# Kernel optimization log

Hardware: AMD Instinct MI355X
Metric: run time of the kernel (lower is better)

## Reference

```python
import jax, jax.numpy as jnp
import numpy as np

E = 8        # num_experts
TOPK = 2     # k
D = 1024     # input/output size
H = 4096     # expert hidden size


def setup_inputs() -> dict:
    key = jax.random.key(0)
    ks = jax.random.split(key, 8)
    s = 0.02
    return {
        "hidden_states": jax.random.normal(ks[0], (2, 2048, D), dtype=jnp.float32),
        "Wr": jax.random.normal(ks[1], (D, E), dtype=jnp.float32) * s,
        "br": jnp.zeros((E,), dtype=jnp.float32),
        "gate_bias": jnp.zeros((E,), dtype=jnp.float32),
        "W1": jax.random.normal(ks[2], (E, D, H), dtype=jnp.float32) * s,
        "b1": jnp.zeros((E, H), dtype=jnp.float32),
        "W2": jax.random.normal(ks[3], (E, H, D), dtype=jnp.float32) * s,
        "b2": jnp.zeros((E, D), dtype=jnp.float32),
    }


def reference(hidden_states, Wr, br, gate_bias, W1, b1, W2, b2):
    B, S, Din = hidden_states.shape
    x = hidden_states.reshape(B * S, Din)              # [T, D]
    # Router: logits + gate bias, top-k, softmax over the k selected logits
    logits = x @ Wr + br + gate_bias                   # [T, E]
    top_v, top_i = jax.lax.top_k(logits, TOPK)         # [T, k]
    probs = jax.nn.softmax(top_v, axis=-1)             # [T, k]
    # Scatter top-k probs into dense per-expert gate weights [T, E]
    gate = jnp.einsum("tk,tke->te", probs,
                      jax.nn.one_hot(top_i, E, dtype=probs.dtype))
    # Per-expert MLP (exact gelu, eval mode -> no dropout/noise),
    # weighted-combine; zero gate weight == token not routed to expert.
    out = jnp.zeros((B * S, W2.shape[-1]), dtype=x.dtype)
    for e in range(E):
        h = jax.nn.gelu(x @ W1[e] + b1[e], approximate=False)  # [T, H]
        y = h @ W2[e] + b2[e]                                  # [T, D]
        out = out + gate[:, e:e + 1] * y
    return out.reshape(B, S, -1)
```

## Files before the change

kernel.cpp:

```cpp
#include <hip/hip_runtime.h>
#include <hip/hip_bf16.h>
#include <stdint.h>
#include <stddef.h>


#define T_TOK 4096
#define DIM   1024
#define HID   4096
#define NE    8
#define MT_MAX 40

typedef unsigned short u16;
typedef __bf16 bf16x8 __attribute__((ext_vector_type(8)));
typedef float  f32x4  __attribute__((ext_vector_type(4)));
typedef u16    u16x8  __attribute__((ext_vector_type(8)));

__device__ __forceinline__ u16 f2bf(float f) {
  union { float f; uint32_t u; } v; v.f = f;
  uint32_t u = v.u;
  return (u16)((u + 0x7fffu + ((u >> 16) & 1u)) >> 16);
}

__device__ __forceinline__ void async_load16(const void* g, void* l) {
  typedef __attribute__((address_space(1))) void GPtr;
  typedef __attribute__((address_space(3))) void LPtr;
  __builtin_amdgcn_global_load_lds((GPtr*)g, (LPtr*)l, 16, 0, 0);
}

__global__ void router_kernel(const float* __restrict__ x, const float* __restrict__ Wr,
                              const float* __restrict__ br, const float* __restrict__ gb,
                              int* __restrict__ counts, int* __restrict__ lists,
                              float* __restrict__ gate_p) {
  const int t = blockIdx.x * 4 + (threadIdx.x >> 6);
  const int lane = threadIdx.x & 63;
  const float* xr = x + (size_t)t * DIM;
  float acc[NE];
#pragma unroll
  for (int e = 0; e < NE; ++e) acc[e] = 0.f;
#pragma unroll
  for (int i = 0; i < DIM / 64; ++i) {
    const int k = i * 64 + lane;
    const float xv = xr[k];
    const float4 w0 = *reinterpret_cast<const float4*>(Wr + (size_t)k * NE);
    const float4 w1 = *reinterpret_cast<const float4*>(Wr + (size_t)k * NE + 4);
    acc[0] += xv * w0.x; acc[1] += xv * w0.y; acc[2] += xv * w0.z; acc[3] += xv * w0.w;
    acc[4] += xv * w1.x; acc[5] += xv * w1.y; acc[6] += xv * w1.z; acc[7] += xv * w1.w;
  }
#pragma unroll
  for (int off = 32; off >= 1; off >>= 1) {
#pragma unroll
    for (int e = 0; e < NE; ++e) acc[e] += __shfl_xor(acc[e], off);
  }
  if (lane == 0) {
    float lg[NE];
#pragma unroll
    for (int e = 0; e < NE; ++e) lg[e] = acc[e] + br[e] + gb[e];
    int i0 = 0;
#pragma unroll
    for (int e = 1; e < NE; ++e) if (lg[e] > lg[i0]) i0 = e;
    int i1 = (i0 == 0) ? 1 : 0;
#pragma unroll
    for (int e = 0; e < NE; ++e) if (e != i0 && lg[e] > lg[i1]) i1 = e;
    const float ev = expf(lg[i1] - lg[i0]);
    const float p0 = 1.f / (1.f + ev);
    const float p1 = ev / (1.f + ev);
    const int pos0 = atomicAdd(&counts[i0], 1);
    lists[i0 * T_TOK + pos0] = t * 2 + 0;
    const int pos1 = atomicAdd(&counts[i1], 1);
    lists[i1 * T_TOK + pos1] = t * 2 + 1;
    gate_p[t * 2 + 0] = p0;
    gate_p[t * 2 + 1] = p1;
  }
}

__global__ void tile_table_kernel(const int* __restrict__ counts, int* __restrict__ tab) {
  if (threadIdx.x == 0) {
    int tot = 0;
    for (int e = 0; e < NE; ++e) {
      const int c = counts[e];
      const int nt = (c + 255) >> 8;
      for (int i = 0; i < nt && tot < MT_MAX; ++i) {
        tab[tot * 2] = e; tab[tot * 2 + 1] = i * 256; ++tot;
      }
    }
    for (; tot < MT_MAX; ++tot) tab[tot * 2] = -1;
  }
}

__global__ void cvt_x_kernel(const float* __restrict__ in, u16* __restrict__ out, int n8) {
  const int i = blockIdx.x * blockDim.x + threadIdx.x;
  if (i >= n8) return;
  const float4 a = reinterpret_cast<const float4*>(in)[2 * i];
  const float4 b = reinterpret_cast<const float4*>(in)[2 * i + 1];
  u16x8 r;
  r[0] = f2bf(a.x); r[1] = f2bf(a.y); r[2] = f2bf(a.z); r[3] = f2bf(a.w);
  r[4] = f2bf(b.x); r[5] = f2bf(b.y); r[6] = f2bf(b.z); r[7] = f2bf(b.w);
  *reinterpret_cast<u16x8*>(out + (size_t)i * 8) = r;
}

__global__ void cvt_w_kernel(const float* __restrict__ in, u16* __restrict__ out,
                             int K, int N) {
  __shared__ float tile[64][65];
  const int e = blockIdx.z;
  const int n0 = blockIdx.x * 64, k0 = blockIdx.y * 64;
  const int tid = threadIdx.x;
  const float* src = in + (size_t)e * K * N;
#pragma unroll
  for (int r = 0; r < 16; ++r) {
    const int kr = r * 4 + (tid >> 6);
    tile[kr][tid & 63] = src[(size_t)(k0 + kr) * N + n0 + (tid & 63)];
  }
  __syncthreads();
  u16* dst = out + (size_t)e * N * K;
#pragma unroll
  for (int r = 0; r < 8; ++r) {
    const int nr = r * 8 + (tid >> 5);
    const int kc = (tid & 31) * 2;
    ushort2 v;
    v.x = f2bf(tile[kc][nr]);
    v.y = f2bf(tile[kc + 1][nr]);
    *reinterpret_cast<ushort2*>(&dst[(size_t)(n0 + nr) * K + k0 + kc]) = v;
  }
}

template <int KT, int NT, int NSPLIT, int PHASE>
__global__ __launch_bounds__(512, 2)
void gemm_kernel(const u16* __restrict__ Abase, const u16* __restrict__ Bt,
                 const float* __restrict__ bias, const int* __restrict__ counts,
                 const int* __restrict__ lists, const float* __restrict__ gate_p,
                 const int* __restrict__ tab,
                 u16* __restrict__ hout, float* __restrict__ yout) {
  const int e = tab[blockIdx.x * 2];
  if (e < 0) return;
  const int m0 = tab[blockIdx.x * 2 + 1];
  const int cnt = counts[e];
  const int n0 = blockIdx.y * 256;
  const int z = blockIdx.z;
  const int kbase = z * (KT / NSPLIT);
  constexpr int nkt = (KT / NSPLIT) / 64;
  constexpr int niter = nkt / 2;

  const int tid = threadIdx.x;
  const int lane = tid & 63, w = tid >> 6;
  const int wm = w >> 2, wn = w & 3;
  const int bh = wn >> 1, bs = wn & 1;
  const int l15 = lane & 15, lks = lane >> 4;

  __shared__ alignas(16) u16 lds[65536];
  __shared__ int rowp[256];

  if (tid < 256) {
    const int idx = m0 + tid;
    rowp[tid] = lists[e * T_TOK + (idx < cnt ? idx : cnt - 1)];
  }
  __syncthreads();

  const int sslot = (tid & 7) ^ ((tid >> 3) & 7);
  const u16* aPtr[2][2];
  const u16* bPtr[2][2];
#pragma unroll
  for (int h = 0; h < 2; ++h)
#pragma unroll
    for (int s = 0; s < 2; ++s) {
      const int r = h * 128 + s * 64 + (tid >> 3);
      const int p = rowp[r];
      const int arow = (PHASE == 1) ? (p >> 1) : p;
      aPtr[h][s] = Abase + (size_t)arow * KT + kbase + sslot * 8;
      bPtr[h][s] = Bt + ((size_t)e * NT + n0 + r) * KT + kbase + sslot * 8;
    }

  int aoff[2];
#pragma unroll
  for (int k = 0; k < 2; ++k)
    aoff[k] = l15 * 64 + (((k * 4 + lks) ^ (l15 & 7)) * 8);

  f32x4 acc[8][4];
#pragma unroll
  for (int a = 0; a < 8; ++a)
#pragma unroll
    for (int b = 0; b < 4; ++b) acc[a][b] = f32x4{0.f, 0.f, 0.f, 0.f};

  bf16x8 af[4][2], bfr[4][2];

#define RDA(C, FMH)                                                            \
  _Pragma("unroll") for (int f_ = 0; f_ < 4; ++f_)                             \
  _Pragma("unroll") for (int k_ = 0; k_ < 2; ++k_)                             \
    af[f_][k_] = *reinterpret_cast<const bf16x8*>(                             \
        &lds[(((C) * 2 + wm) * 2 + (FMH)) * 4096 + f_ * 1024 + aoff[k_]]);

#define RDB(C)                                                                 \
  _Pragma("unroll") for (int g_ = 0; g_ < 4; ++g_)                             \
  _Pragma("unroll") for (int k_ = 0; k_ < 2; ++k_)                             \
    bfr[g_][k_] = *reinterpret_cast<const bf16x8*>(                            \
        &lds[32768 + (((C) * 2 + bh) * 2 + bs) * 4096 + g_ * 1024 + aoff[k_]]);

#define SGA(C, S, TT)                                                          \
  _Pragma("unroll") for (int h_ = 0; h_ < 2; ++h_)                             \
    async_load16(aPtr[h_][S] + (TT) * 64,                                      \
                 &lds[(((C) * 2 + h_) * 2 + (S)) * 4096 + w * 512]);

#define SGB(C, H, TT)                                                          \
  _Pragma("unroll") for (int s_ = 0; s_ < 2; ++s_)                             \
    async_load16(bPtr[H][s_] + (TT) * 64,                                      \
                 &lds[32768 + (((C) * 2 + (H)) * 2 + s_) * 4096 + w * 512]);

#define MMQ(FMH, FNH)                                                          \
  _Pragma("unroll") for (int f_ = 0; f_ < 4; ++f_)                             \
  _Pragma("unroll") for (int g_ = 0; g_ < 2; ++g_)                             \
  _Pragma("unroll") for (int k_ = 0; k_ < 2; ++k_)                             \
    acc[(FMH) * 4 + f_][(FNH) * 2 + g_] =                                      \
        __builtin_amdgcn_mfma_f32_16x16x32_bf16(                               \
            af[f_][k_], bfr[(FNH) * 2 + g_][k_],                               \
            acc[(FMH) * 4 + f_][(FNH) * 2 + g_], 0, 0, 0);

#define CORE(FMH, FNH)                                                         \
  __builtin_amdgcn_s_barrier();                                                \
  asm volatile("s_waitcnt lgkmcnt(0)" ::: "memory");                           \
  __builtin_amdgcn_sched_barrier(0);                                           \
  __builtin_amdgcn_s_setprio(1);                                               \
  MMQ(FMH, FNH);                                                               \
  __builtin_amdgcn_s_setprio(0);                                               \
  __builtin_amdgcn_sched_barrier(0);

#define BAR() __builtin_amdgcn_s_barrier();

#define ITER(T, LAST)                                                          \
  {                                                                            \
    RDA(0, 0); RDB(0);                                                         \
    SGA(1, 1, (T) + 1);                                 \
    CORE(0, 0) BAR()                                                           \
    if (!(LAST)) { SGA(0, 0, (T) + 2); }                \
    CORE(0, 1) BAR()                                                           \
    RDA(0, 1);                                                                 \
    if (!(LAST)) { SGB(0, 0, (T) + 2); }                        \
    CORE(1, 0) BAR()                                                           \
    if (!(LAST)) { SGB(0, 1, (T) + 2); }                        \
    CORE(1, 1)                                                                 \
    if (LAST) { asm volatile("s_waitcnt vmcnt(0)" ::: "memory"); }             \
    else      { asm volatile("s_waitcnt vmcnt(6)" ::: "memory"); }             \
    __builtin_amdgcn_sched_barrier(0);                                         \
    BAR()                                                                      \
    RDA(1, 0); RDB(1);                                                         \
    if (!(LAST)) { SGA(0, 1, (T) + 2); }                        \
    CORE(0, 0) BAR()                                                           \
    if (!(LAST)) { SGA(1, 0, (T) + 3); }                \
    CORE(0, 1) BAR()                                                           \
    RDA(1, 1);                                                                 \
    if (!(LAST)) { SGB(1, 0, (T) + 3); }                        \
    CORE(1, 0) BAR()                                                           \
    if (!(LAST)) { SGB(1, 1, (T) + 3); }                        \
    CORE(1, 1)                                                                 \
    if (!(LAST)) {                                                             \
      asm volatile("s_waitcnt vmcnt(6)" ::: "memory");                         \
      __builtin_amdgcn_sched_barrier(0);                                       \
    }                                                                          \
    BAR()                                                                      \
  }

  SGA(0, 0, 0); SGB(0, 0, 0); SGB(0, 1, 0); SGA(0, 1, 0);
  SGA(1, 0, 1); SGB(1, 0, 1); SGB(1, 1, 1);
  asm volatile("s_waitcnt vmcnt(6)" ::: "memory");
  __builtin_amdgcn_sched_barrier(0);
  __builtin_amdgcn_s_barrier();

  for (int it = 0; it < niter - 1; ++it) {
    const int t = 2 * it;
    ITER(t, false);
  }
  ITER(nkt - 2, true);

#undef ITER
#undef CORE
#undef MMQ
#undef SGB
#undef SGA
#undef RDB
#undef RDA
#undef BAR

  const float* bias_e = bias + (size_t)e * NT;
  const float bz = (z == 0) ? 1.f : 0.f;
#pragma unroll
  for (int fm = 0; fm < 8; ++fm) {
    const int rbase = wm * 128 + (fm >> 2) * 64 + (fm & 3) * 16 + (lane >> 4) * 4;
#pragma unroll
    for (int r = 0; r < 4; ++r) {
      const int row = rbase + r;
      if (m0 + row >= cnt) continue;
      const int p = rowp[row];
#pragma unroll
      for (int nf = 0; nf < 4; ++nf) {
        const int n = n0 + wn * 64 + nf * 16 + l15;
        const float v = acc[fm][nf][r];
        if (PHASE == 1) {
          const float vb = v + bias_e[n];
          const float g = 0.5f * vb * (1.0f + erff(vb * 0.70710678118654752f));
          hout[(size_t)p * NT + n] = f2bf(g);
        } else if (PHASE == 2) {
          yout[(size_t)z * T_TOK * 2 * NT + (size_t)p * NT + n] =
              gate_p[p] * (v + bz * bias_e[n]);
        } else {
          atomicAdd(&yout[(size_t)(p >> 1) * NT + n], gate_p[p] * (v + bz * bias_e[n]));
        }
      }
    }
  }
}

__global__ void combine4_kernel(const float* __restrict__ yp, float* __restrict__ out) {
  const int i = blockIdx.x * blockDim.x + threadIdx.x;
  const int t = i >> 8, d4 = i & 255;
  const size_t r0 = (size_t)(2 * t) * 256 + d4;
  const size_t zoff = (size_t)T_TOK * 2 * DIM / 4;
  const float4 a = reinterpret_cast<const float4*>(yp)[r0];
  const float4 b = reinterpret_cast<const float4*>(yp)[r0 + 256];
  const float4 c = reinterpret_cast<const float4*>(yp)[zoff + r0];
  const float4 d = reinterpret_cast<const float4*>(yp)[zoff + r0 + 256];
  float4 o;
  o.x = a.x + b.x + c.x + d.x; o.y = a.y + b.y + c.y + d.y;
  o.z = a.z + b.z + c.z + d.z; o.w = a.w + b.w + c.w + d.w;
  reinterpret_cast<float4*>(out)[i] = o;
}

extern "C" void kernel_launch(void* const* d_in, const int* in_sizes, int n_in,
                              void* d_out, int out_size, void* d_ws, size_t ws_size,
                              hipStream_t stream) {
  const float* x  = (const float*)d_in[0];
  const float* Wr = (const float*)d_in[1];
  const float* br = (const float*)d_in[2];
  const float* gb = (const float*)d_in[3];
  const float* W1 = (const float*)d_in[4];
  const float* b1 = (const float*)d_in[5];
  const float* W2 = (const float*)d_in[6];
  const float* b2 = (const float*)d_in[7];
  float* out = (float*)d_out;

  char* ws = (char*)d_ws;
  size_t off = 0;
  int*   counts = (int*)(ws + off);   off += 256;
  int*   ttab   = (int*)(ws + off);   off += 512;
  int*   lists  = (int*)(ws + off);   off += (size_t)NE * T_TOK * 4;
  float* gate_p = (float*)(ws + off); off += (size_t)T_TOK * 2 * 4;
  u16*   xb     = (u16*)(ws + off);   off += (size_t)T_TOK * DIM * 2;
  u16*   wbuf   = (u16*)(ws + off);   off += (size_t)NE * DIM * HID * 2;
  u16*   hbuf   = (u16*)(ws + off);   off += (size_t)T_TOK * 2 * HID * 2;
  float* ypair  = (float*)(ws + off);
  const size_t need_full = off + (size_t)2 * T_TOK * 2 * DIM * 4;
  const bool use_ypair = (ws_size >= need_full);

  hipMemsetAsync(counts, 0, 32, stream);
  router_kernel<<<T_TOK / 4, 256, 0, stream>>>(x, Wr, br, gb, counts, lists, gate_p);
  tile_table_kernel<<<1, 64, 0, stream>>>(counts, ttab);
  cvt_x_kernel<<<(T_TOK * DIM / 8 + 255) / 256, 256, 0, stream>>>(x, xb, T_TOK * DIM / 8);
  cvt_w_kernel<<<dim3(HID / 64, DIM / 64, NE), 256, 0, stream>>>(W1, wbuf, DIM, HID);
  gemm_kernel<DIM, HID, 1, 1><<<dim3(MT_MAX, HID / 256, 1), 512, 0, stream>>>(
      xb, wbuf, b1, counts, lists, gate_p, ttab, hbuf, nullptr);
  cvt_w_kernel<<<dim3(DIM / 64, HID / 64, NE), 256, 0, stream>>>(W2, wbuf, HID, DIM);
  if (use_ypair) {
    gemm_kernel<HID, DIM, 2, 2><<<dim3(MT_MAX, DIM / 256, 2), 512, 0, stream>>>(
        hbuf, wbuf, b2, counts, lists, gate_p, ttab, nullptr, ypair);
    combine4_kernel<<<T_TOK * DIM / 4 / 256, 256, 0, stream>>>(ypair, out);
  } else {
    hipMemsetAsync(out, 0, (size_t)out_size * 4, stream);
    gemm_kernel<HID, DIM, 2, 3><<<dim3(MT_MAX, DIM / 256, 2), 512, 0, stream>>>(
        hbuf, wbuf, b2, counts, lists, gate_p, ttab, nullptr, out);
  }
}
```

Before: 497.9 us.

## Store GEMM operands in K-slab-major layout of 64-wide column blocks

Activations, converted weights and the hidden buffer are now stored as 64-wide K slabs, each slab holding all rows contiguously (row*64 within a slab). The GEMM address math and async loads step by one whole slab per K tile instead of 64 elements along a long row. Each 16-byte load group now reads 128 contiguous bytes per row, and rows sit next to each other. This is meant to improve DRAM page and TLB locality for the gathered, routed rows and the weight tiles. The converters and the phase-1 epilogue write in this layout. That scatters the stores more widely and spreads each tile's loads across many distant slabs.

```diff
diff --git a/kernel.cpp b/kernel.cpp
--- a/kernel.cpp
+++ b/kernel.cpp
@@ -87,15 +87,17 @@
   }
 }
 
-__global__ void cvt_x_kernel(const float* __restrict__ in, u16* __restrict__ out, int n8) {
+__global__ void cvt_x_kernel(const float* __restrict__ in, u16* __restrict__ out) {
   const int i = blockIdx.x * blockDim.x + threadIdx.x;
-  if (i >= n8) return;
-  const float4 a = reinterpret_cast<const float4*>(in)[2 * i];
-  const float4 b = reinterpret_cast<const float4*>(in)[2 * i + 1];
+  const int t = i >> 7;
+  const int d0 = (i & 127) * 8;
+  const float4 a = *reinterpret_cast<const float4*>(in + (size_t)t * DIM + d0);
+  const float4 b = *reinterpret_cast<const float4*>(in + (size_t)t * DIM + d0 + 4);
   u16x8 r;
   r[0] = f2bf(a.x); r[1] = f2bf(a.y); r[2] = f2bf(a.z); r[3] = f2bf(a.w);
   r[4] = f2bf(b.x); r[5] = f2bf(b.y); r[6] = f2bf(b.z); r[7] = f2bf(b.w);
-  *reinterpret_cast<u16x8*>(out + (size_t)i * 8) = r;
+  *reinterpret_cast<u16x8*>(out + (size_t)(d0 >> 6) * (T_TOK * 64) +
+                            (size_t)t * 64 + (d0 & 63)) = r;
 }
 
 __global__ void cvt_w_kernel(const float* __restrict__ in, u16* __restrict__ out,
@@ -111,7 +113,7 @@
     tile[kr][tid & 63] = src[(size_t)(k0 + kr) * N + n0 + (tid & 63)];
   }
   __syncthreads();
-  u16* dst = out + (size_t)e * N * K;
+  u16* dst = out + (size_t)e * K * N + (size_t)(k0 >> 6) * ((size_t)N * 64);
 #pragma unroll
   for (int r = 0; r < 8; ++r) {
     const int nr = r * 8 + (tid >> 5);
@@ -119,7 +121,7 @@
     ushort2 v;
     v.x = f2bf(tile[kc][nr]);
     v.y = f2bf(tile[kc + 1][nr]);
-    *reinterpret_cast<ushort2*>(&dst[(size_t)(n0 + nr) * K + k0 + kc]) = v;
+    *reinterpret_cast<ushort2*>(&dst[(size_t)(n0 + nr) * 64 + kc]) = v;
   }
 }
 
@@ -136,9 +138,12 @@
   const int cnt = counts[e];
   const int n0 = blockIdx.y * 256;
   const int z = blockIdx.z;
-  const int kbase = z * (KT / NSPLIT);
+  const int kb64 = z * ((KT / NSPLIT) / 64);
   constexpr int nkt = (KT / NSPLIT) / 64;
   constexpr int niter = nkt / 2;
+  constexpr size_t AKT = (PHASE == 1) ? (size_t)T_TOK * 64 : (size_t)T_TOK * 2 * 64;
+  constexpr size_t BKT = (size_t)NT * 64;
+  constexpr size_t HSLAB = (size_t)T_TOK * 2 * 64;
 
   const int tid = threadIdx.x;
   const int lane = tid & 63, w = tid >> 6;
@@ -165,8 +170,9 @@
       const int r = h * 128 + s * 64 + (tid >> 3);
       const int p = rowp[r];
       const int arow = (PHASE == 1) ? (p >> 1) : p;
-      aPtr[h][s] = Abase + (size_t)arow * KT + kbase + sslot * 8;
-      bPtr[h][s] = Bt + ((size_t)e * NT + n0 + r) * KT + kbase + sslot * 8;
+      aPtr[h][s] = Abase + (size_t)kb64 * AKT + (size_t)arow * 64 + sslot * 8;
+      bPtr[h][s] = Bt + (size_t)e * NT * KT + (size_t)kb64 * BKT +
+                   (size_t)(n0 + r) * 64 + sslot * 8;
     }
 
   int aoff[2];
@@ -196,12 +202,12 @@
 
 #define SGA(C, S, TT)                                                          \
   _Pragma("unroll") for (int h_ = 0; h_ < 2; ++h_)                             \
-    async_load16(aPtr[h_][S] + (TT) * 64,                                      \
+    async_load16(aPtr[h_][S] + (size_t)(TT) * AKT,                             \
                  &lds[(((C) * 2 + h_) * 2 + (S)) * 4096 + w * 512]);
 
 #define SGB(C, H, TT)                                                          \
   _Pragma("unroll") for (int s_ = 0; s_ < 2; ++s_)                             \
-    async_load16(bPtr[H][s_] + (TT) * 64,                                      \
+    async_load16(bPtr[H][s_] + (size_t)(TT) * BKT,                             \
                  &lds[32768 + (((C) * 2 + (H)) * 2 + s_) * 4096 + w * 512]);
 
 #define MMQ(FMH, FNH)                                                          \
@@ -227,28 +233,28 @@
 #define ITER(T, LAST)                                                          \
   {                                                                            \
     RDA(0, 0); RDB(0);                                                         \
-    SGA(1, 1, (T) + 1);                                 \
+    SGA(1, 1, (T) + 1);                                                        \
     CORE(0, 0) BAR()                                                           \
-    if (!(LAST)) { SGA(0, 0, (T) + 2); }                \
+    if (!(LAST)) { SGA(0, 0, (T) + 2); }                                       \
     CORE(0, 1) BAR()                                                           \
     RDA(0, 1);                                                                 \
-    if (!(LAST)) { SGB(0, 0, (T) + 2); }                        \
+    if (!(LAST)) { SGB(0, 0, (T) + 2); }                                       \
     CORE(1, 0) BAR()                                                           \
-    if (!(LAST)) { SGB(0, 1, (T) + 2); }                        \
+    if (!(LAST)) { SGB(0, 1, (T) + 2); }                                       \
     CORE(1, 1)                                                                 \
     if (LAST) { asm volatile("s_waitcnt vmcnt(0)" ::: "memory"); }             \
     else      { asm volatile("s_waitcnt vmcnt(6)" ::: "memory"); }             \
     __builtin_amdgcn_sched_barrier(0);                                         \
     BAR()                                                                      \
     RDA(1, 0); RDB(1);                                                         \
-    if (!(LAST)) { SGA(0, 1, (T) + 2); }                        \
+    if (!(LAST)) { SGA(0, 1, (T) + 2); }                                       \
     CORE(0, 0) BAR()                                                           \
-    if (!(LAST)) { SGA(1, 0, (T) + 3); }                \
+    if (!(LAST)) { SGA(1, 0, (T) + 3); }                                       \
     CORE(0, 1) BAR()                                                           \
     RDA(1, 1);                                                                 \
-    if (!(LAST)) { SGB(1, 0, (T) + 3); }                        \
+    if (!(LAST)) { SGB(1, 0, (T) + 3); }                                       \
     CORE(1, 0) BAR()                                                           \
-    if (!(LAST)) { SGB(1, 1, (T) + 3); }                        \
+    if (!(LAST)) { SGB(1, 1, (T) + 3); }                                       \
     CORE(1, 1)                                                                 \
     if (!(LAST)) {                                                             \
       asm volatile("s_waitcnt vmcnt(6)" ::: "memory");                         \
@@ -295,7 +301,7 @@
         if (PHASE == 1) {
           const float vb = v + bias_e[n];
           const float g = 0.5f * vb * (1.0f + erff(vb * 0.70710678118654752f));
-          hout[(size_t)p * NT + n] = f2bf(g);
+          hout[(size_t)(n >> 6) * HSLAB + (size_t)p * 64 + (n & 63)] = f2bf(g);
         } else if (PHASE == 2) {
           yout[(size_t)z * T_TOK * 2 * NT + (size_t)p * NT + n] =
               gate_p[p] * (v + bz * bias_e[n]);
@@ -351,7 +357,7 @@
   hipMemsetAsync(counts, 0, 32, stream);
   router_kernel<<<T_TOK / 4, 256, 0, stream>>>(x, Wr, br, gb, counts, lists, gate_p);
   tile_table_kernel<<<1, 64, 0, stream>>>(counts, ttab);
-  cvt_x_kernel<<<(T_TOK * DIM / 8 + 255) / 256, 256, 0, stream>>>(x, xb, T_TOK * DIM / 8);
+  cvt_x_kernel<<<T_TOK * DIM / 8 / 256, 256, 0, stream>>>(x, xb);
   cvt_w_kernel<<<dim3(HID / 64, DIM / 64, NE), 256, 0, stream>>>(W1, wbuf, DIM, HID);
   gemm_kernel<DIM, HID, 1, 1><<<dim3(MT_MAX, HID / 256, 1), 512, 0, stream>>>(
       xb, wbuf, b1, counts, lists, gate_p, ttab, hbuf, nullptr);
```

Result: slower. 508.0 us (+2.0%).
